# Optimization experiments

Hardware: AMD Instinct MI355X
Metric: run time of the kernel (lower is better)

The kernel has to match this reference:

```python
import jax, jax.numpy as jnp
import numpy as np

N_NODES = 50000
N_EDGES = 800000
IN_CH = 128
HID = 16
HEADS = 8
OUT_CH = 40
NEG_SLOPE = 0.2  # PyG GATConv default leaky_relu slope


def segment_softmax(logits, seg, num_segments):
    # logits: [E, H], softmax over edges sharing the same destination node
    m = jax.ops.segment_max(logits, seg, num_segments=num_segments)  # [N, H]
    e = jnp.exp(logits - m[seg])
    s = jax.ops.segment_sum(e, seg, num_segments=num_segments)  # [N, H]
    return e / s[seg]


def gat_conv(x, edge_index, W, att_src, att_dst, bias, heads, ch, concat):
    N = x.shape[0]
    h = (x @ W).reshape(N, heads, ch)                     # [N, H, C]
    a_src = jnp.sum(h * att_src, axis=-1)                 # [N, H]
    a_dst = jnp.sum(h * att_dst, axis=-1)                 # [N, H]
    src, dst = edge_index[0], edge_index[1]
    alpha = jax.nn.leaky_relu(a_src[src] + a_dst[dst], NEG_SLOPE)  # [E, H]
    alpha = segment_softmax(alpha, dst, N)                # [E, H]
    msg = h[src] * alpha[:, :, None]                      # [E, H, C]
    out = jax.ops.segment_sum(msg, dst, num_segments=N)   # [N, H, C]
    out = out.reshape(N, heads * ch) if concat else out.mean(axis=1)
    return out + bias


def setup_inputs() -> dict:
    key = jax.random.key(0)
    ks = jax.random.split(key, 10)
    g = 0.1
    return {
        "x": jax.random.normal(ks[0], (N_NODES, IN_CH), jnp.float32),
        "edge_index": jax.random.randint(ks[1], (2, N_EDGES), 0, N_NODES, jnp.int32),
        "W1": jax.random.normal(ks[2], (IN_CH, HEADS * HID), jnp.float32) * g,
        "att_src1": jax.random.normal(ks[3], (HEADS, HID), jnp.float32) * g,
        "att_dst1": jax.random.normal(ks[4], (HEADS, HID), jnp.float32) * g,
        "b1": jnp.zeros((HEADS * HID,), jnp.float32),
        "W2": jax.random.normal(ks[5], (HEADS * HID, OUT_CH), jnp.float32) * g,
        "att_src2": jax.random.normal(ks[6], (1, OUT_CH), jnp.float32) * g,
        "att_dst2": jax.random.normal(ks[7], (1, OUT_CH), jnp.float32) * g,
        "b2": jnp.zeros((OUT_CH,), jnp.float32),
    }


def reference(x, edge_index, W1, att_src1, att_dst1, b1, W2, att_src2, att_dst2, b2):
    # layer 1: GATConv(in->hid, heads=8, concat) + ELU (dropout is identity in eval)
    h = gat_conv(x, edge_index, W1, att_src1, att_dst1, b1, HEADS, HID, concat=True)
    h = jax.nn.elu(h)
    # layer 2: GATConv(hid*heads->out, heads=1, concat=False)
    out = gat_conv(h, edge_index, W2, att_src2, att_dst2, b2, 1, OUT_CH, concat=False)
    return out
```

## Files before the change

### kernel.cpp

```cpp
#include <hip/hip_runtime.h>
#include <hip/hip_bf16.h>
#include <math.h>

#define N_NODES 50000
#define E_EDGES 800000
#define IN_CH 128
#define HIDX 128
#define OUT_CH 40
#define NEG_SLOPE 0.2f
#define SCAN_NBLK ((N_NODES + 1023) / 1024)

static __device__ __forceinline__ unsigned int f2bf_pk(float lo, float hi) {
    unsigned int ul = __float_as_uint(lo);
    unsigned int uh = __float_as_uint(hi);
    ul = (ul + 0x7fffu + ((ul >> 16) & 1u)) >> 16;
    uh = (uh + 0x7fffu + ((uh >> 16) & 1u)) >> 16;
    return ul | (uh << 16);
}
static __device__ __forceinline__ float bf2f(unsigned short u) {
    return __uint_as_float(((unsigned int)u) << 16);
}


__global__ void zero_kernel(int* __restrict__ p, int n) {
    int i = blockIdx.x * blockDim.x + threadIdx.x;
    if (i < n) p[i] = 0;
}

__global__ void rank_hist_kernel(const int* __restrict__ ei, int* __restrict__ deg,
                                 int* __restrict__ rank) {
    int i = blockIdx.x * blockDim.x + threadIdx.x;
    if (i < E_EDGES) {
        int d = ei[E_EDGES + i];
        rank[i] = atomicAdd(&deg[d], 1);
    }
}

__global__ __launch_bounds__(1024) void scan1_kernel(const int* __restrict__ deg,
                                                     int* __restrict__ rowptr,
                                                     int* __restrict__ bsum) {
    __shared__ int wsum[16];
    __shared__ int woff[16];
    int tid = threadIdx.x;
    int lane = tid & 63, wid = tid >> 6;
    int i = blockIdx.x * 1024 + tid;
    int v = (i < N_NODES) ? deg[i] : 0;
    int orig = v;
#pragma unroll
    for (int off = 1; off < 64; off <<= 1) {
        int t = __shfl_up(v, off);
        if (lane >= off) v += t;
    }
    if (lane == 63) wsum[wid] = v;
    __syncthreads();
    if (wid == 0) {
        int wv = (lane < 16) ? wsum[lane] : 0;
#pragma unroll
        for (int off = 1; off < 16; off <<= 1) {
            int t = __shfl_up(wv, off);
            if (lane >= off) wv += t;
        }
        if (lane < 16) woff[lane] = wv;
    }
    __syncthreads();
    int wbase = (wid == 0) ? 0 : woff[wid - 1];
    if (i < N_NODES) rowptr[i] = wbase + v - orig;
    if (tid == 0) bsum[blockIdx.x] = woff[15];
}

__global__ void scan2_kernel(int* __restrict__ bsum) {
    int lane = threadIdx.x;
    int v = (lane < SCAN_NBLK) ? bsum[lane] : 0;
    int orig = v;
#pragma unroll
    for (int off = 1; off < 64; off <<= 1) {
        int t = __shfl_up(v, off);
        if (lane >= off) v += t;
    }
    if (lane < SCAN_NBLK) bsum[lane] = v - orig;
}

__global__ __launch_bounds__(1024) void scan3_kernel(int* __restrict__ rowptr,
                                                     const int* __restrict__ bsum) {
    int i = blockIdx.x * 1024 + threadIdx.x;
    if (i < N_NODES) rowptr[i] += bsum[blockIdx.x];
    if (i == 0) rowptr[N_NODES] = E_EDGES;
}

__global__ void scatter_kernel(const int* __restrict__ ei, const int* __restrict__ rowptr,
                               const int* __restrict__ rank, int* __restrict__ csr_src) {
    int i = blockIdx.x * blockDim.x + threadIdx.x;
    if (i < E_EDGES) {
        int d = ei[E_EDGES + i];
        int pos = rowptr[d] + rank[i];
        csr_src[pos] = ei[i];
    }
}


__global__ __launch_bounds__(256) void gemm1_kernel(
    const float* __restrict__ x, const float* __restrict__ W1,
    const float* __restrict__ as1, const float* __restrict__ ad1,
    unsigned short* __restrict__ H1, float* __restrict__ A1s, float* __restrict__ A1d)
{
    __shared__ float Ws[128 * 68];
    __shared__ float XT[64 * 132];
    int tid = threadIdx.x;
    int rowbase = blockIdx.x * 64;
    int cb = blockIdx.y;

    const float4* W4 = (const float4*)W1;
#pragma unroll
    for (int i = 0; i < 8; i++) {
        int f = i * 256 + tid;
        int k = f >> 4, c4 = f & 15;
        *(float4*)(Ws + k * 68 + c4 * 4) = W4[k * 32 + cb * 16 + c4];
    }
    const float4* x4 = (const float4*)x;
#pragma unroll
    for (int i = 0; i < 8; i++) {
        int f = i * 256 + tid;
        int r = f >> 5, c4 = f & 31;
        int gr = rowbase + r; if (gr >= N_NODES) gr = N_NODES - 1;
        *(float4*)(XT + r * 132 + c4 * 4) = x4[gr * 32 + c4];
    }
    __syncthreads();

    int cg = tid & 15;
    int rg = tid >> 4;
    int c0 = cg * 4;
    int r0 = rg * 4;
    float acc[4][4];
#pragma unroll
    for (int i = 0; i < 4; i++)
#pragma unroll
        for (int j = 0; j < 4; j++) acc[i][j] = 0.f;

    for (int k = 0; k < 128; k += 4) {
        float4 xv[4];
#pragma unroll
        for (int i = 0; i < 4; i++) xv[i] = *(const float4*)(XT + (r0 + i) * 132 + k);
#pragma unroll
        for (int kk = 0; kk < 4; kk++) {
            float4 wv = *(const float4*)(Ws + (k + kk) * 68 + c0);
#pragma unroll
            for (int i = 0; i < 4; i++) {
                float xs = (kk == 0) ? xv[i].x : (kk == 1) ? xv[i].y : (kk == 2) ? xv[i].z : xv[i].w;
                acc[i][0] += xs * wv.x; acc[i][1] += xs * wv.y;
                acc[i][2] += xs * wv.z; acc[i][3] += xs * wv.w;
            }
        }
    }

    int gc0 = cb * 64 + c0;
    int hh = gc0 >> 4;
    float asp[4] = {0, 0, 0, 0}, adp[4] = {0, 0, 0, 0};
#pragma unroll
    for (int j = 0; j < 4; j++) {
        float va = as1[gc0 + j];
        float vd = ad1[gc0 + j];
#pragma unroll
        for (int i = 0; i < 4; i++) { asp[i] += acc[i][j] * va; adp[i] += acc[i][j] * vd; }
    }
#pragma unroll
    for (int i = 0; i < 4; i++) {
        asp[i] += __shfl_xor(asp[i], 1); asp[i] += __shfl_xor(asp[i], 2);
        adp[i] += __shfl_xor(adp[i], 1); adp[i] += __shfl_xor(adp[i], 2);
    }
#pragma unroll
    for (int i = 0; i < 4; i++) {
        int gr = rowbase + r0 + i;
        if (gr < N_NODES) {
            uint2 v;
            v.x = f2bf_pk(acc[i][0], acc[i][1]);
            v.y = f2bf_pk(acc[i][2], acc[i][3]);
            *(uint2*)(H1 + gr * 128 + gc0) = v;
            if ((cg & 3) == 0) {
                A1s[gr * 8 + hh] = asp[i];
                A1d[gr * 8 + hh] = adp[i];
            }
        }
    }
}


__global__ __launch_bounds__(256) void agg1_kernel(
    const int* __restrict__ rowptr, const int* __restrict__ csr_src,
    const float* __restrict__ A1s, const float* __restrict__ A1d,
    const unsigned short* __restrict__ H1, const float* __restrict__ b1,
    float* __restrict__ X2)
{
    int gwave = (blockIdx.x * blockDim.x + threadIdx.x) >> 6;
    int lane = threadIdx.x & 63;
    if (gwave >= N_NODES) return;
    int node = gwave;
    int beg = rowptr[node], end = rowptr[node + 1];
    int half = lane >> 5;
    int li = lane & 31;
    int head = li >> 2;
    int c0 = li * 4;
    float ad = A1d[node * 8 + head];
    float acc0 = 0.f, acc1 = 0.f, acc2 = 0.f, acc3 = 0.f, sumw = 0.f;
    int p = beg;
    for (; p + 8 <= end; p += 8) {
        int s0 = csr_src[p + half];
        int s1 = csr_src[p + 2 + half];
        int s2 = csr_src[p + 4 + half];
        int s3 = csr_src[p + 6 + half];
        float a0 = A1s[s0 * 8 + head];
        float a1 = A1s[s1 * 8 + head];
        float a2 = A1s[s2 * 8 + head];
        float a3 = A1s[s3 * 8 + head];
        ushort4 u0 = *(const ushort4*)(H1 + s0 * 128 + c0);
        ushort4 u1 = *(const ushort4*)(H1 + s1 * 128 + c0);
        ushort4 u2 = *(const ushort4*)(H1 + s2 * 128 + c0);
        ushort4 u3 = *(const ushort4*)(H1 + s3 * 128 + c0);
        float z0 = a0 + ad; z0 = z0 >= 0.f ? z0 : NEG_SLOPE * z0; float w0 = __expf(z0);
        float z1 = a1 + ad; z1 = z1 >= 0.f ? z1 : NEG_SLOPE * z1; float w1 = __expf(z1);
        float z2 = a2 + ad; z2 = z2 >= 0.f ? z2 : NEG_SLOPE * z2; float w2 = __expf(z2);
        float z3 = a3 + ad; z3 = z3 >= 0.f ? z3 : NEG_SLOPE * z3; float w3 = __expf(z3);
        acc0 += w0 * bf2f(u0.x) + w1 * bf2f(u1.x) + w2 * bf2f(u2.x) + w3 * bf2f(u3.x);
        acc1 += w0 * bf2f(u0.y) + w1 * bf2f(u1.y) + w2 * bf2f(u2.y) + w3 * bf2f(u3.y);
        acc2 += w0 * bf2f(u0.z) + w1 * bf2f(u1.z) + w2 * bf2f(u2.z) + w3 * bf2f(u3.z);
        acc3 += w0 * bf2f(u0.w) + w1 * bf2f(u1.w) + w2 * bf2f(u2.w) + w3 * bf2f(u3.w);
        sumw += w0 + w1 + w2 + w3;
    }
    for (; p + 4 <= end; p += 4) {
        int s0 = csr_src[p + half];
        int s1 = csr_src[p + 2 + half];
        float a0 = A1s[s0 * 8 + head];
        float a1 = A1s[s1 * 8 + head];
        ushort4 u0 = *(const ushort4*)(H1 + s0 * 128 + c0);
        ushort4 u1 = *(const ushort4*)(H1 + s1 * 128 + c0);
        float z0 = a0 + ad; z0 = z0 >= 0.f ? z0 : NEG_SLOPE * z0; float w0 = __expf(z0);
        float z1 = a1 + ad; z1 = z1 >= 0.f ? z1 : NEG_SLOPE * z1; float w1 = __expf(z1);
        acc0 += w0 * bf2f(u0.x) + w1 * bf2f(u1.x);
        acc1 += w0 * bf2f(u0.y) + w1 * bf2f(u1.y);
        acc2 += w0 * bf2f(u0.z) + w1 * bf2f(u1.z);
        acc3 += w0 * bf2f(u0.w) + w1 * bf2f(u1.w);
        sumw += w0 + w1;
    }
    for (; p < end; p += 2) {
        int e = p + half;
        bool valid = e < end;
        int s = csr_src[valid ? e : beg];
        float a = A1s[s * 8 + head];
        ushort4 u = *(const ushort4*)(H1 + s * 128 + c0);
        float z = a + ad; z = z >= 0.f ? z : NEG_SLOPE * z;
        float w = valid ? __expf(z) : 0.f;
        acc0 += w * bf2f(u.x);
        acc1 += w * bf2f(u.y);
        acc2 += w * bf2f(u.z);
        acc3 += w * bf2f(u.w);
        sumw += w;
    }
    acc0 += __shfl_xor(acc0, 32);
    acc1 += __shfl_xor(acc1, 32);
    acc2 += __shfl_xor(acc2, 32);
    acc3 += __shfl_xor(acc3, 32);
    sumw += __shfl_xor(sumw, 32);
    if (half == 0) {
        float inv = (end > beg) ? 1.0f / sumw : 0.0f;
        float4 bv = *(const float4*)(b1 + c0);
        float o0 = acc0 * inv + bv.x;
        float o1 = acc1 * inv + bv.y;
        float o2 = acc2 * inv + bv.z;
        float o3 = acc3 * inv + bv.w;
        o0 = o0 > 0.f ? o0 : expm1f(o0);
        o1 = o1 > 0.f ? o1 : expm1f(o1);
        o2 = o2 > 0.f ? o2 : expm1f(o2);
        o3 = o3 > 0.f ? o3 : expm1f(o3);
        float4 ov = {o0, o1, o2, o3};
        *(float4*)(X2 + node * 128 + c0) = ov;
    }
}


__global__ __launch_bounds__(256) void gemm2_kernel(
    const float* __restrict__ X2, const float* __restrict__ W2,
    const float* __restrict__ as2, const float* __restrict__ ad2,
    unsigned short* __restrict__ H2, float* __restrict__ A2s, float* __restrict__ A2d)
{
    __shared__ float Ws[128 * 40];
    __shared__ float XS[64 * 132];
    int tid = threadIdx.x;
    int rowbase = blockIdx.x * 64;

#pragma unroll
    for (int i = 0; i < 20; i++) Ws[i * 256 + tid] = W2[i * 256 + tid];

    const float4* x4 = (const float4*)X2;
#pragma unroll
    for (int i = 0; i < 8; i++) {
        int f = i * 256 + tid;
        int r = f >> 5, c4 = f & 31;
        int gr = rowbase + r; if (gr >= N_NODES) gr = N_NODES - 1;
        *(float4*)(XS + r * 132 + c4 * 4) = x4[gr * 32 + c4];
    }
    __syncthreads();

    int q = tid & 3, r = tid >> 2;
    float acc[10];
#pragma unroll
    for (int j = 0; j < 10; j++) acc[j] = 0.f;
    for (int k = 0; k < 128; k += 4) {
        float4 xv = *(const float4*)(XS + r * 132 + k);
#pragma unroll
        for (int kk = 0; kk < 4; kk++) {
            float xs = (kk == 0) ? xv.x : (kk == 1) ? xv.y : (kk == 2) ? xv.z : xv.w;
#pragma unroll
            for (int j = 0; j < 10; j++) acc[j] += xs * Ws[(k + kk) * 40 + q * 10 + j];
        }
    }
    float asum = 0.f, dsum = 0.f;
#pragma unroll
    for (int j = 0; j < 10; j++) {
        asum += acc[j] * as2[q * 10 + j];
        dsum += acc[j] * ad2[q * 10 + j];
    }
    asum += __shfl_xor(asum, 1); asum += __shfl_xor(asum, 2);
    dsum += __shfl_xor(dsum, 1); dsum += __shfl_xor(dsum, 2);
    int gr = rowbase + r;
    if (gr < N_NODES) {
#pragma unroll
        for (int t = 0; t < 5; t++)
            *(unsigned int*)(H2 + gr * 40 + q * 10 + t * 2) = f2bf_pk(acc[t * 2], acc[t * 2 + 1]);
        if (q == 0) { A2s[gr] = asum; A2d[gr] = dsum; }
    }
}


__global__ __launch_bounds__(256) void agg2_kernel(
    const int* __restrict__ rowptr, const int* __restrict__ csr_src,
    const float* __restrict__ A2s, const float* __restrict__ A2d,
    const unsigned short* __restrict__ H2, const float* __restrict__ b2,
    float* __restrict__ out)
{
    int gwave = (blockIdx.x * blockDim.x + threadIdx.x) >> 6;
    int lane = threadIdx.x & 63;
    if (gwave >= N_NODES) return;
    int node = gwave;
    int beg = rowptr[node], end = rowptr[node + 1];
    int half = lane >> 5;
    int li = lane & 31;
    bool act = li < 20;
    int c0 = li * 2;
    int cc = act ? c0 : 0;
    float ad = A2d[node];
    float acc0 = 0.f, acc1 = 0.f, sumw = 0.f;
    int p = beg;
    for (; p + 8 <= end; p += 8) {
        int s0 = csr_src[p + half];
        int s1 = csr_src[p + 2 + half];
        int s2 = csr_src[p + 4 + half];
        int s3 = csr_src[p + 6 + half];
        float a0 = A2s[s0];
        float a1 = A2s[s1];
        float a2 = A2s[s2];
        float a3 = A2s[s3];
        ushort2 u0 = *(const ushort2*)(H2 + s0 * OUT_CH + cc);
        ushort2 u1 = *(const ushort2*)(H2 + s1 * OUT_CH + cc);
        ushort2 u2 = *(const ushort2*)(H2 + s2 * OUT_CH + cc);
        ushort2 u3 = *(const ushort2*)(H2 + s3 * OUT_CH + cc);
        float z0 = a0 + ad; z0 = z0 >= 0.f ? z0 : NEG_SLOPE * z0; float w0 = __expf(z0);
        float z1 = a1 + ad; z1 = z1 >= 0.f ? z1 : NEG_SLOPE * z1; float w1 = __expf(z1);
        float z2 = a2 + ad; z2 = z2 >= 0.f ? z2 : NEG_SLOPE * z2; float w2 = __expf(z2);
        float z3 = a3 + ad; z3 = z3 >= 0.f ? z3 : NEG_SLOPE * z3; float w3 = __expf(z3);
        acc0 += w0 * bf2f(u0.x) + w1 * bf2f(u1.x) + w2 * bf2f(u2.x) + w3 * bf2f(u3.x);
        acc1 += w0 * bf2f(u0.y) + w1 * bf2f(u1.y) + w2 * bf2f(u2.y) + w3 * bf2f(u3.y);
        sumw += w0 + w1 + w2 + w3;
    }
    for (; p + 4 <= end; p += 4) {
        int s0 = csr_src[p + half];
        int s1 = csr_src[p + 2 + half];
        float a0 = A2s[s0];
        float a1 = A2s[s1];
        ushort2 u0 = *(const ushort2*)(H2 + s0 * OUT_CH + cc);
        ushort2 u1 = *(const ushort2*)(H2 + s1 * OUT_CH + cc);
        float z0 = a0 + ad; z0 = z0 >= 0.f ? z0 : NEG_SLOPE * z0; float w0 = __expf(z0);
        float z1 = a1 + ad; z1 = z1 >= 0.f ? z1 : NEG_SLOPE * z1; float w1 = __expf(z1);
        acc0 += w0 * bf2f(u0.x) + w1 * bf2f(u1.x);
        acc1 += w0 * bf2f(u0.y) + w1 * bf2f(u1.y);
        sumw += w0 + w1;
    }
    for (; p < end; p += 2) {
        int e = p + half;
        bool valid = e < end;
        int s = csr_src[valid ? e : beg];
        float a = A2s[s];
        ushort2 u = *(const ushort2*)(H2 + s * OUT_CH + cc);
        float z = a + ad; z = z >= 0.f ? z : NEG_SLOPE * z;
        float w = valid ? __expf(z) : 0.f;
        acc0 += w * bf2f(u.x);
        acc1 += w * bf2f(u.y);
        sumw += w;
    }
    acc0 += __shfl_xor(acc0, 32);
    acc1 += __shfl_xor(acc1, 32);
    sumw += __shfl_xor(sumw, 32);
    if (half == 0 && act) {
        float inv = (end > beg) ? 1.0f / sumw : 0.0f;
        float o0 = acc0 * inv + b2[c0];
        float o1 = acc1 * inv + b2[c0 + 1];
        float2 ov = {o0, o1};
        *(float2*)(out + node * OUT_CH + c0) = ov;
    }
}


extern "C" void kernel_launch(void* const* d_in, const int* in_sizes, int n_in,
                              void* d_out, int out_size, void* d_ws, size_t ws_size,
                              hipStream_t stream) {
    const float* x   = (const float*)d_in[0];
    const int*   ei  = (const int*)d_in[1];
    const float* W1  = (const float*)d_in[2];
    const float* as1 = (const float*)d_in[3];
    const float* ad1 = (const float*)d_in[4];
    const float* b1  = (const float*)d_in[5];
    const float* W2  = (const float*)d_in[6];
    const float* as2 = (const float*)d_in[7];
    const float* ad2 = (const float*)d_in[8];
    const float* b2  = (const float*)d_in[9];
    float* out = (float*)d_out;

    char* ws = (char*)d_ws;
    size_t off = 0;
    auto alloc = [&](size_t bytes) {
        void* p = ws + off;
        off += (bytes + 255) & ~size_t(255);
        return p;
    };
    unsigned short* H1 = (unsigned short*)alloc((size_t)N_NODES * 128 * 2);
    float* X2     = (float*)alloc((size_t)N_NODES * 128 * 4);
    unsigned short* H2 = (unsigned short*)alloc((size_t)N_NODES * OUT_CH * 2);
    float* A1s    = (float*)alloc((size_t)N_NODES * 8 * 4);
    float* A1d    = (float*)alloc((size_t)N_NODES * 8 * 4);
    float* A2s    = (float*)alloc((size_t)N_NODES * 4);
    float* A2d    = (float*)alloc((size_t)N_NODES * 4);
    int* deg      = (int*)alloc((size_t)N_NODES * 4);
    int* rowptr   = (int*)alloc((size_t)(N_NODES + 1) * 4);
    int* rank     = (int*)alloc((size_t)E_EDGES * 4);
    int* csr_src  = (int*)alloc((size_t)E_EDGES * 4);
    int* bsum     = (int*)alloc((size_t)SCAN_NBLK * 4);

    zero_kernel<<<(N_NODES + 255) / 256, 256, 0, stream>>>(deg, N_NODES);
    rank_hist_kernel<<<(E_EDGES + 255) / 256, 256, 0, stream>>>(ei, deg, rank);
    scan1_kernel<<<SCAN_NBLK, 1024, 0, stream>>>(deg, rowptr, bsum);
    scan2_kernel<<<1, 64, 0, stream>>>(bsum);
    scan3_kernel<<<SCAN_NBLK, 1024, 0, stream>>>(rowptr, bsum);
    scatter_kernel<<<(E_EDGES + 255) / 256, 256, 0, stream>>>(ei, rowptr, rank, csr_src);

    dim3 g1((N_NODES + 63) / 64, 2);
    gemm1_kernel<<<g1, 256, 0, stream>>>(x, W1, as1, ad1, H1, A1s, A1d);
    agg1_kernel<<<(N_NODES + 3) / 4, 256, 0, stream>>>(rowptr, csr_src, A1s, A1d, H1, b1, X2);

    gemm2_kernel<<<(N_NODES + 63) / 64, 256, 0, stream>>>(X2, W2, as2, ad2, H2, A2s, A2d);
    agg2_kernel<<<(N_NODES + 3) / 4, 256, 0, stream>>>(rowptr, csr_src, A2s, A2d, H2, b2, out);
}
```

Before: 264.2 us.

## Fuse degree histogram into gemm1, merge scan passes, unroll aggregation deeper

The per-edge degree histogram with atomic rank assignment moves into the first GEMM kernel, so it no longer needs its own launch. The block-sum scan is folded into the final scan kernel, with each block recomputing the prefix through a wave shuffle. Both aggregation kernels gain a 16-edge unrolled loop that issues eight gathers per half-wave before accumulating, to expose more memory parallelism. The trade-offs are higher register pressure in the aggregation kernels and atomic traffic added to the GEMM blocks.

```diff
diff --git a/kernel.cpp b/kernel.cpp
--- a/kernel.cpp
+++ b/kernel.cpp
@@ -25,15 +25,6 @@
 __global__ void zero_kernel(int* __restrict__ p, int n) {
     int i = blockIdx.x * blockDim.x + threadIdx.x;
     if (i < n) p[i] = 0;
-}
-
-__global__ void rank_hist_kernel(const int* __restrict__ ei, int* __restrict__ deg,
-                                 int* __restrict__ rank) {
-    int i = blockIdx.x * blockDim.x + threadIdx.x;
-    if (i < E_EDGES) {
-        int d = ei[E_EDGES + i];
-        rank[i] = atomicAdd(&deg[d], 1);
-    }
 }
 
 __global__ __launch_bounds__(1024) void scan1_kernel(const int* __restrict__ deg,
@@ -68,22 +59,23 @@
     if (tid == 0) bsum[blockIdx.x] = woff[15];
 }
 
-__global__ void scan2_kernel(int* __restrict__ bsum) {
-    int lane = threadIdx.x;
-    int v = (lane < SCAN_NBLK) ? bsum[lane] : 0;
-    int orig = v;
-#pragma unroll
-    for (int off = 1; off < 64; off <<= 1) {
-        int t = __shfl_up(v, off);
-        if (lane >= off) v += t;
-    }
-    if (lane < SCAN_NBLK) bsum[lane] = v - orig;
-}
-
 __global__ __launch_bounds__(1024) void scan3_kernel(int* __restrict__ rowptr,
                                                      const int* __restrict__ bsum) {
-    int i = blockIdx.x * 1024 + threadIdx.x;
-    if (i < N_NODES) rowptr[i] += bsum[blockIdx.x];
+    __shared__ int sbase;
+    int tid = threadIdx.x;
+    if (tid < 64) {
+        int v = (tid < SCAN_NBLK) ? bsum[tid] : 0;
+#pragma unroll
+        for (int off = 1; off < 64; off <<= 1) {
+            int t = __shfl_up(v, off);
+            if (tid >= off) v += t;
+        }
+        int pre = __shfl(v, blockIdx.x - 1);
+        if (tid == 0) sbase = (blockIdx.x == 0) ? 0 : pre;
+    }
+    __syncthreads();
+    int i = blockIdx.x * 1024 + tid;
+    if (i < N_NODES) rowptr[i] += sbase;
     if (i == 0) rowptr[N_NODES] = E_EDGES;
 }
 
@@ -101,13 +93,26 @@
 __global__ __launch_bounds__(256) void gemm1_kernel(
     const float* __restrict__ x, const float* __restrict__ W1,
     const float* __restrict__ as1, const float* __restrict__ ad1,
-    unsigned short* __restrict__ H1, float* __restrict__ A1s, float* __restrict__ A1d)
+    unsigned short* __restrict__ H1, float* __restrict__ A1s, float* __restrict__ A1d,
+    const int* __restrict__ ei, int* __restrict__ deg, int* __restrict__ rank)
 {
     __shared__ float Ws[128 * 68];
     __shared__ float XT[64 * 132];
     int tid = threadIdx.x;
     int rowbase = blockIdx.x * 64;
     int cb = blockIdx.y;
+
+    {
+        int ebase = (blockIdx.y * gridDim.x + blockIdx.x) * 512 + tid;
+#pragma unroll
+        for (int t = 0; t < 2; t++) {
+            int e = ebase + t * 256;
+            if (e < E_EDGES) {
+                int d = ei[E_EDGES + e];
+                rank[e] = atomicAdd(&deg[d], 1);
+            }
+        }
+    }
 
     const float4* W4 = (const float4*)W1;
 #pragma unroll
@@ -202,6 +207,25 @@
     float ad = A1d[node * 8 + head];
     float acc0 = 0.f, acc1 = 0.f, acc2 = 0.f, acc3 = 0.f, sumw = 0.f;
     int p = beg;
+    for (; p + 16 <= end; p += 16) {
+        int s[8]; float a[8]; ushort4 u[8];
+#pragma unroll
+        for (int t = 0; t < 8; t++) s[t] = csr_src[p + 2 * t + half];
+#pragma unroll
+        for (int t = 0; t < 8; t++) a[t] = A1s[s[t] * 8 + head];
+#pragma unroll
+        for (int t = 0; t < 8; t++) u[t] = *(const ushort4*)(H1 + s[t] * 128 + c0);
+#pragma unroll
+        for (int t = 0; t < 8; t++) {
+            float z = a[t] + ad; z = z >= 0.f ? z : NEG_SLOPE * z;
+            float w = __expf(z);
+            acc0 += w * bf2f(u[t].x);
+            acc1 += w * bf2f(u[t].y);
+            acc2 += w * bf2f(u[t].z);
+            acc3 += w * bf2f(u[t].w);
+            sumw += w;
+        }
+    }
     for (; p + 8 <= end; p += 8) {
         int s0 = csr_src[p + half];
         int s1 = csr_src[p + 2 + half];
@@ -349,6 +373,23 @@
     float ad = A2d[node];
     float acc0 = 0.f, acc1 = 0.f, sumw = 0.f;
     int p = beg;
+    for (; p + 16 <= end; p += 16) {
+        int s[8]; float a[8]; ushort2 u[8];
+#pragma unroll
+        for (int t = 0; t < 8; t++) s[t] = csr_src[p + 2 * t + half];
+#pragma unroll
+        for (int t = 0; t < 8; t++) a[t] = A2s[s[t]];
+#pragma unroll
+        for (int t = 0; t < 8; t++) u[t] = *(const ushort2*)(H2 + s[t] * OUT_CH + cc);
+#pragma unroll
+        for (int t = 0; t < 8; t++) {
+            float z = a[t] + ad; z = z >= 0.f ? z : NEG_SLOPE * z;
+            float w = __expf(z);
+            acc0 += w * bf2f(u[t].x);
+            acc1 += w * bf2f(u[t].y);
+            sumw += w;
+        }
+    }
     for (; p + 8 <= end; p += 8) {
         int s0 = csr_src[p + half];
         int s1 = csr_src[p + 2 + half];
@@ -444,14 +485,14 @@
     int* bsum     = (int*)alloc((size_t)SCAN_NBLK * 4);
 
     zero_kernel<<<(N_NODES + 255) / 256, 256, 0, stream>>>(deg, N_NODES);
-    rank_hist_kernel<<<(E_EDGES + 255) / 256, 256, 0, stream>>>(ei, deg, rank);
+
+    dim3 g1((N_NODES + 63) / 64, 2);
+    gemm1_kernel<<<g1, 256, 0, stream>>>(x, W1, as1, ad1, H1, A1s, A1d, ei, deg, rank);
+
     scan1_kernel<<<SCAN_NBLK, 1024, 0, stream>>>(deg, rowptr, bsum);
-    scan2_kernel<<<1, 64, 0, stream>>>(bsum);
     scan3_kernel<<<SCAN_NBLK, 1024, 0, stream>>>(rowptr, bsum);
     scatter_kernel<<<(E_EDGES + 255) / 256, 256, 0, stream>>>(ei, rowptr, rank, csr_src);
 
-    dim3 g1((N_NODES + 63) / 64, 2);
-    gemm1_kernel<<<g1, 256, 0, stream>>>(x, W1, as1, ad1, H1, A1s, A1d);
     agg1_kernel<<<(N_NODES + 3) / 4, 256, 0, stream>>>(rowptr, csr_src, A1s, A1d, H1, b1, X2);
 
     gemm2_kernel<<<(N_NODES + 63) / 64, 256, 0, stream>>>(X2, W2, as2, ad2, H2, A2s, A2d);
```

Result: faster. 246.0 us (-6.9%).
